# Kernel tuning notes

Measured on AMD Instinct MI355X. Metric: run time of the kernel, lower is better.

Reference implementation:

```python
import jax, jax.numpy as jnp
import numpy as np

N = 8192      # nodes
D_IN = 128    # input features
D_H = 48      # GAT hidden (hardcoded in module)
D_OUT = 32    # control output dim
NEG_INF = -9e15  # matches torch code's -9000000000000000.0


def setup_inputs() -> dict:
    key = jax.random.key(0)
    ks = jax.random.split(key, 12)
    s = 0.05
    return {
        "x": jax.random.normal(ks[0], (N, D_IN), jnp.float32),
        "adj": jax.random.randint(ks[1], (N, N), 0, 2, jnp.int32),
        "W_gat": jax.random.normal(ks[2], (D_H, D_IN), jnp.float32) * s,
        "a": jax.random.normal(ks[3], (1, D_H), jnp.float32) * s,
        "gamma": jnp.ones((D_H,), jnp.float32),
        "beta": jnp.zeros((D_H,), jnp.float32),
        "W1": jax.random.normal(ks[4], (256, D_H), jnp.float32) * s,
        "b1": jnp.zeros((256,), jnp.float32),
        "W2": jax.random.normal(ks[5], (128, 256), jnp.float32) * s,
        "b2": jnp.zeros((128,), jnp.float32),
        "W3": jax.random.normal(ks[6], (D_OUT, 128), jnp.float32) * s,
        "b3": jnp.zeros((D_OUT,), jnp.float32),
    }


def reference(x, adj, W_gat, a, gamma, beta, W1, b1, W2, b2, W3, b3):
    # --- LightweightGATLayer ---
    Wh = x @ W_gat.T                      # [N, D_H]
    s = Wh @ a.T                          # [N, 1] additive attention scores
    e = s + s.T                           # [N, N]
    e = jnp.where(e > 0, e, 0.2 * e)      # LeakyReLU(0.2)
    e = jnp.where(adj > 0, e, NEG_INF)    # mask non-edges
    attn = jax.nn.softmax(e, axis=1)      # row softmax; dropout is identity in eval
    h_prime = attn @ Wh                   # [N, D_H]
    # LayerNorm over last dim, eps=1e-5
    mu = jnp.mean(h_prime, axis=-1, keepdims=True)
    var = jnp.var(h_prime, axis=-1, keepdims=True)
    h = (h_prime - mu) * jax.lax.rsqrt(var + 1e-5) * gamma + beta
    # --- BiACT MLP head: 48 -> 256 -> 128 -> D_OUT ---
    h = jax.nn.relu(h @ W1.T + b1)
    h = jax.nn.relu(h @ W2.T + b2)
    return h @ W3.T + b3                  # [N, D_OUT]
```

## Files before the change

### kernel.cpp

```cpp
#include <hip/hip_runtime.h>

#define N 8192
#define DIN 128
#define DH 48
#define MT 128
#define KC 64
#define PSTR (KC + 8)
#define NSPLIT 8
#define JSPAN (N / NSPLIT)
#define NCHUNK (JSPAN / KC)
#define ACC_STRIDE 64
#define RB 32

typedef _Float16 half8 __attribute__((ext_vector_type(8)));
typedef float f32x4 __attribute__((ext_vector_type(4)));

__global__ __launch_bounds__(256) void k_wh(const float* __restrict__ x,
                                            const float* __restrict__ Wg,
                                            float* __restrict__ Wh) {
    __shared__ float wT[DIN * DH];
    int t = threadIdx.x;
    for (int e = t; e < DIN * DH; e += 256) {
        int c = e / DIN, k = e % DIN;
        wT[k * DH + c] = Wg[e];
    }
    __syncthreads();
    int o = blockIdx.x * 256 + t;
    int r = o / DH, c = o % DH;
    const float4* xr = (const float4*)(x + (size_t)r * DIN);
    float acc = 0.f;
    #pragma unroll 8
    for (int k4 = 0; k4 < DIN / 4; ++k4) {
        float4 xv = xr[k4];
        int kb = k4 * 4;
        acc += xv.x * wT[(kb + 0) * DH + c];
        acc += xv.y * wT[(kb + 1) * DH + c];
        acc += xv.z * wT[(kb + 2) * DH + c];
        acc += xv.w * wT[(kb + 3) * DH + c];
    }
    Wh[o] = acc;
}

__global__ __launch_bounds__(256) void k_s(const float* __restrict__ Wh,
                                           const float* __restrict__ a,
                                           float* __restrict__ s) {
    int r = blockIdx.x * 256 + threadIdx.x;
    const float4* wr = (const float4*)(Wh + (size_t)r * DH);
    const float4* av = (const float4*)a;
    float acc = 0.f;
    #pragma unroll
    for (int k4 = 0; k4 < DH / 4; ++k4) {
        float4 w = wr[k4]; float4 aa = av[k4];
        acc += w.x * aa.x + w.y * aa.y + w.z * aa.z + w.w * aa.w;
    }
    s[r] = acc;
}

__global__ __launch_bounds__(256) void k_gat(const int* __restrict__ adj,
                                             const float* __restrict__ Wh,
                                             const float* __restrict__ s,
                                             float* __restrict__ accWs) {
    __shared__ _Float16 pS[MT][PSTR];
    __shared__ _Float16 wS[64][PSTR];
    __shared__ float sRow[MT];
    int t = threadIdx.x;
    int tile = blockIdx.x & 63;
    int split = blockIdx.x >> 6;
    int i0 = tile * MT;
    int jbase = split * JSPAN;

    int lane = t & 63, w = t >> 6;
    int ln16 = lane & 15, kq = lane >> 4;
    int jp = t & 31, rg = t >> 5;

    const int* adjBase = adj + (size_t)(i0 + rg * 16) * N + jbase + 2 * jp;

    int2 adjR[16];
    float whR[12];
    #pragma unroll
    for (int it = 0; it < 16; ++it)
        adjR[it] = *(const int2*)(adjBase + (size_t)it * N);
    #pragma unroll
    for (int k = 0; k < 12; ++k)
        whR[k] = Wh[(size_t)jbase * DH + t + k * 256];

    if (t < MT) sRow[t] = s[i0 + t];
    for (int e = t; e < 16 * PSTR; e += 256) {
        int n = 48 + e / PSTR, k = e % PSTR;
        wS[n][k] = (n == 48) ? (_Float16)1.0f : (_Float16)0.0f;
    }

    f32x4 acc[2][4];
    #pragma unroll
    for (int a0 = 0; a0 < 2; ++a0)
        #pragma unroll
        for (int b0 = 0; b0 < 4; ++b0) acc[a0][b0] = (f32x4){0.f, 0.f, 0.f, 0.f};

    __syncthreads();

    for (int chunk = 0; chunk < NCHUNK; ++chunk) {
        int j0 = jbase + chunk * KC;
        #pragma unroll
        for (int k = 0; k < 12; ++k) {
            int e = t + k * 256;
            int jc = e / DH, d = e % DH;
            wS[d][jc] = (_Float16)whR[k];
        }
        {
            float2 sj = *(const float2*)(s + j0 + 2 * jp);
            #pragma unroll
            for (int it = 0; it < 16; ++it) {
                int r = rg * 16 + it;
                int2 av = adjR[it];
                float e0 = sRow[r] + sj.x;
                float e1 = sRow[r] + sj.y;
                e0 = fmaxf(e0, 0.2f * e0);
                e1 = fmaxf(e1, 0.2f * e1);
                float p0 = av.x ? __expf(e0) : 0.f;
                float p1 = av.y ? __expf(e1) : 0.f;
                union { _Float16 h[2]; unsigned u; } pk;
                pk.h[0] = (_Float16)p0;
                pk.h[1] = (_Float16)p1;
                *(unsigned*)&pS[r][2 * jp] = pk.u;
            }
        }
        if (chunk < NCHUNK - 1) {
            int jn = j0 + KC;
            #pragma unroll
            for (int it = 0; it < 16; ++it)
                adjR[it] = *(const int2*)(adjBase + (size_t)it * N + (chunk + 1) * KC);
            #pragma unroll
            for (int k = 0; k < 12; ++k)
                whR[k] = Wh[(size_t)jn * DH + t + k * 256];
        }
        __syncthreads();
        {
            const int m0 = w * 32;
            #pragma unroll
            for (int kt = 0; kt < 2; ++kt) {
                const int kk = kt * 32 + kq * 8;
                half8 b[4];
                #pragma unroll
                for (int nt = 0; nt < 4; ++nt)
                    b[nt] = *(const half8*)&wS[nt * 16 + ln16][kk];
                #pragma unroll
                for (int mtl = 0; mtl < 2; ++mtl) {
                    half8 a = *(const half8*)&pS[m0 + mtl * 16 + ln16][kk];
                    #pragma unroll
                    for (int nt = 0; nt < 4; ++nt)
                        acc[mtl][nt] = __builtin_amdgcn_mfma_f32_16x16x32_f16(
                            a, b[nt], acc[mtl][nt], 0, 0, 0);
                }
            }
        }
        __syncthreads();
    }
    size_t rbase = (size_t)split * N + i0;
    #pragma unroll
    for (int mtl = 0; mtl < 2; ++mtl) {
        #pragma unroll
        for (int nt = 0; nt < 4; ++nt) {
            int col = nt * 16 + ln16;
            if (nt == 3 && ln16 != 0) continue;
            #pragma unroll
            for (int reg = 0; reg < 4; ++reg) {
                int row = w * 32 + mtl * 16 + kq * 4 + reg;
                accWs[(rbase + row) * ACC_STRIDE + col] = acc[mtl][nt][reg];
            }
        }
    }
}

__global__ __launch_bounds__(256) void k_mlp(const float* __restrict__ accWs,
                                             const float* __restrict__ gamma,
                                             const float* __restrict__ beta,
                                             const float* __restrict__ W1, const float* __restrict__ b1,
                                             const float* __restrict__ W2, const float* __restrict__ b2,
                                             const float* __restrict__ W3, const float* __restrict__ b3,
                                             float* __restrict__ out) {
    __shared__ float hacc[RB * 49];
    __shared__ _Float16 hN[RB * 72];
    __shared__ _Float16 h1[RB * 264];
    __shared__ float h2[RB * 132];
    int t = threadIdx.x;
    int r0 = blockIdx.x * RB;
    int lane = t & 63, w = t >> 6;
    int ln16 = lane & 15, kq = lane >> 4;

    for (int e = t; e < RB * 49; e += 256) {
        int r = e / 49, d = e % 49;
        size_t base = (size_t)(r0 + r) * ACC_STRIDE + d;
        float v = 0.f;
        #pragma unroll
        for (int sp = 0; sp < NSPLIT; ++sp)
            v += accWs[(size_t)sp * N * ACC_STRIDE + base];
        hacc[e] = v;
    }
    __syncthreads();

    if (t < RB) {
        float invl = 1.f / hacc[t * 49 + 48];
        float sum = 0.f;
        for (int d = 0; d < DH; ++d) sum += hacc[t * 49 + d];
        float mean = sum * invl * (1.f / DH);
        float var = 0.f;
        for (int d = 0; d < DH; ++d) {
            float dv = hacc[t * 49 + d] * invl - mean;
            var += dv * dv;
        }
        var *= (1.f / DH);
        float rs = rsqrtf(var + 1e-5f);
        for (int d = 0; d < DH; ++d) {
            float hv = (hacc[t * 49 + d] * invl - mean) * rs;
            hN[t * 72 + d] = (_Float16)(hv * gamma[d] + beta[d]);
        }
        for (int d = DH; d < 72; ++d) hN[t * 72 + d] = (_Float16)0.f;
    }
    __syncthreads();

    {
        f32x4 acc1[2][4];
        #pragma unroll
        for (int mt = 0; mt < 2; ++mt)
            #pragma unroll
            for (int nt = 0; nt < 4; ++nt) acc1[mt][nt] = (f32x4){0.f, 0.f, 0.f, 0.f};
        #pragma unroll
        for (int kt = 0; kt < 2; ++kt) {
            int k = kt * 32 + kq * 8;
            half8 a[2];
            #pragma unroll
            for (int mt = 0; mt < 2; ++mt)
                a[mt] = *(const half8*)&hN[(mt * 16 + ln16) * 72 + k];
            #pragma unroll
            for (int ntl = 0; ntl < 4; ++ntl) {
                int n = (w * 4 + ntl) * 16 + ln16;
                half8 b;
                #pragma unroll
                for (int i = 0; i < 8; ++i) b[i] = (_Float16)0.f;
                if (k < DH) {
                    float4 lo = *(const float4*)(W1 + n * DH + k);
                    float4 hi = *(const float4*)(W1 + n * DH + k + 4);
                    b[0] = (_Float16)lo.x; b[1] = (_Float16)lo.y;
                    b[2] = (_Float16)lo.z; b[3] = (_Float16)lo.w;
                    b[4] = (_Float16)hi.x; b[5] = (_Float16)hi.y;
                    b[6] = (_Float16)hi.z; b[7] = (_Float16)hi.w;
                }
                #pragma unroll
                for (int mt = 0; mt < 2; ++mt)
                    acc1[mt][ntl] = __builtin_amdgcn_mfma_f32_16x16x32_f16(
                        a[mt], b, acc1[mt][ntl], 0, 0, 0);
            }
        }
        #pragma unroll
        for (int mt = 0; mt < 2; ++mt)
            #pragma unroll
            for (int ntl = 0; ntl < 4; ++ntl) {
                int col = (w * 4 + ntl) * 16 + ln16;
                float bias = b1[col];
                #pragma unroll
                for (int reg = 0; reg < 4; ++reg) {
                    int row = mt * 16 + kq * 4 + reg;
                    float v = acc1[mt][ntl][reg] + bias;
                    h1[row * 264 + col] = (_Float16)fmaxf(v, 0.f);
                }
            }
    }
    __syncthreads();

    {
        f32x4 acc2[2][2];
        #pragma unroll
        for (int mt = 0; mt < 2; ++mt)
            #pragma unroll
            for (int nt = 0; nt < 2; ++nt) acc2[mt][nt] = (f32x4){0.f, 0.f, 0.f, 0.f};
        #pragma unroll
        for (int kt = 0; kt < 8; ++kt) {
            int k = kt * 32 + kq * 8;
            half8 a[2];
            #pragma unroll
            for (int mt = 0; mt < 2; ++mt)
                a[mt] = *(const half8*)&h1[(mt * 16 + ln16) * 264 + k];
            #pragma unroll
            for (int ntl = 0; ntl < 2; ++ntl) {
                int n = (w * 2 + ntl) * 16 + ln16;
                float4 lo = *(const float4*)(W2 + n * 256 + k);
                float4 hi = *(const float4*)(W2 + n * 256 + k + 4);
                half8 b;
                b[0] = (_Float16)lo.x; b[1] = (_Float16)lo.y;
                b[2] = (_Float16)lo.z; b[3] = (_Float16)lo.w;
                b[4] = (_Float16)hi.x; b[5] = (_Float16)hi.y;
                b[6] = (_Float16)hi.z; b[7] = (_Float16)hi.w;
                #pragma unroll
                for (int mt = 0; mt < 2; ++mt)
                    acc2[mt][ntl] = __builtin_amdgcn_mfma_f32_16x16x32_f16(
                        a[mt], b, acc2[mt][ntl], 0, 0, 0);
            }
        }
        #pragma unroll
        for (int mt = 0; mt < 2; ++mt)
            #pragma unroll
            for (int ntl = 0; ntl < 2; ++ntl) {
                int col = (w * 2 + ntl) * 16 + ln16;
                float bias = b2[col];
                #pragma unroll
                for (int reg = 0; reg < 4; ++reg) {
                    int row = mt * 16 + kq * 4 + reg;
                    h2[row * 132 + col] = fmaxf(acc2[mt][ntl][reg] + bias, 0.f);
                }
            }
    }
    __syncthreads();

    {
        int c = t & 31;
        int g = t >> 5;
        int rb = g * 4;
        float acc[4];
        float bias = b3[c];
        #pragma unroll
        for (int r = 0; r < 4; ++r) acc[r] = bias;
        const float4* wrow = (const float4*)(W3 + c * 128);
        for (int k4 = 0; k4 < 32; ++k4) {
            float4 wv = wrow[k4];
            #pragma unroll
            for (int r = 0; r < 4; ++r) {
                const float4 hv = *(const float4*)(&h2[(rb + r) * 132 + k4 * 4]);
                acc[r] += wv.x * hv.x + wv.y * hv.y + wv.z * hv.z + wv.w * hv.w;
            }
        }
        #pragma unroll
        for (int r = 0; r < 4; ++r)
            out[(size_t)(r0 + rb + r) * 32 + c] = acc[r];
    }
}

extern "C" void kernel_launch(void* const* d_in, const int* in_sizes, int n_in,
                              void* d_out, int out_size, void* d_ws, size_t ws_size,
                              hipStream_t stream) {
    const float* x     = (const float*)d_in[0];
    const int*   adj   = (const int*)d_in[1];
    const float* Wg    = (const float*)d_in[2];
    const float* a     = (const float*)d_in[3];
    const float* gamma = (const float*)d_in[4];
    const float* beta  = (const float*)d_in[5];
    const float* W1    = (const float*)d_in[6];
    const float* b1    = (const float*)d_in[7];
    const float* W2    = (const float*)d_in[8];
    const float* b2    = (const float*)d_in[9];
    const float* W3    = (const float*)d_in[10];
    const float* b3    = (const float*)d_in[11];
    float* out = (float*)d_out;

    float* ws = (float*)d_ws;
    float* Wh    = ws;
    float* s     = ws + (size_t)N * DH;
    float* accWs = s + N;

    k_wh<<<N * DH / 256, 256, 0, stream>>>(x, Wg, Wh);
    k_s<<<N / 256, 256, 0, stream>>>(Wh, a, s);
    k_gat<<<64 * NSPLIT, 256, 0, stream>>>(adj, Wh, s, accWs);
    k_mlp<<<N / RB, 256, 0, stream>>>(accWs, gamma, beta, W1, b1, W2, b2, W3, b3, out);
}
```

Baseline: 467.0 us.

## Make GAT waves independent using a pre-transposed fp16 Wh and no block barriers

A new kernel writes Wh transposed to fp16, padded to 64 feature rows, with a row of ones that yields the softmax denominator. The GAT kernel now loads its MFMA B fragments straight from global memory instead of staging them in shared memory. Each wave computes and reads only its own 32 rows of attention probabilities, so both per-chunk __syncthreads are gone. The j-dimension split is doubled to 16 and launch bounds request 3 blocks per CU, for more parallelism and better latency hiding. The cost is an extra launch, redundant B-fragment loads per wave, and a partial-sum workspace and reduction in the MLP kernel that are twice as large.

```diff
diff --git a/kernel.cpp b/kernel.cpp
--- a/kernel.cpp
+++ b/kernel.cpp
@@ -6,7 +6,7 @@
 #define MT 128
 #define KC 64
 #define PSTR (KC + 8)
-#define NSPLIT 8
+#define NSPLIT 16
 #define JSPAN (N / NSPLIT)
 #define NCHUNK (JSPAN / KC)
 #define ACC_STRIDE 64
@@ -56,12 +56,22 @@
     s[r] = acc;
 }
 
-__global__ __launch_bounds__(256) void k_gat(const int* __restrict__ adj,
-                                             const float* __restrict__ Wh,
-                                             const float* __restrict__ s,
-                                             float* __restrict__ accWs) {
+__global__ __launch_bounds__(256) void k_tr(const float* __restrict__ Wh,
+                                            _Float16* __restrict__ WhT16) {
+    int o = blockIdx.x * 256 + threadIdx.x;
+    int d = o >> 13, j = o & 8191;
+    _Float16 v;
+    if (d < DH)       v = (_Float16)Wh[(size_t)j * DH + d];
+    else if (d == DH) v = (_Float16)1.0f;
+    else              v = (_Float16)0.0f;
+    WhT16[o] = v;
+}
+
+__global__ __launch_bounds__(256, 3) void k_gat(const int* __restrict__ adj,
+                                                const _Float16* __restrict__ WhT16,
+                                                const float* __restrict__ s,
+                                                float* __restrict__ accWs) {
     __shared__ _Float16 pS[MT][PSTR];
-    __shared__ _Float16 wS[64][PSTR];
     __shared__ float sRow[MT];
     int t = threadIdx.x;
     int tile = blockIdx.x & 63;
@@ -71,24 +81,17 @@
 
     int lane = t & 63, w = t >> 6;
     int ln16 = lane & 15, kq = lane >> 4;
-    int jp = t & 31, rg = t >> 5;
-
-    const int* adjBase = adj + (size_t)(i0 + rg * 16) * N + jbase + 2 * jp;
+    int jp = lane & 31, rh = lane >> 5;
+
+    int rw = w * 32;
+    const int* adjBase = adj + (size_t)(i0 + rw + rh * 16) * N + jbase + 2 * jp;
+
+    if (lane < 32) sRow[rw + lane] = s[i0 + rw + lane];
 
     int2 adjR[16];
-    float whR[12];
     #pragma unroll
     for (int it = 0; it < 16; ++it)
         adjR[it] = *(const int2*)(adjBase + (size_t)it * N);
-    #pragma unroll
-    for (int k = 0; k < 12; ++k)
-        whR[k] = Wh[(size_t)jbase * DH + t + k * 256];
-
-    if (t < MT) sRow[t] = s[i0 + t];
-    for (int e = t; e < 16 * PSTR; e += 256) {
-        int n = 48 + e / PSTR, k = e % PSTR;
-        wS[n][k] = (n == 48) ? (_Float16)1.0f : (_Float16)0.0f;
-    }
 
     f32x4 acc[2][4];
     #pragma unroll
@@ -96,21 +99,20 @@
         #pragma unroll
         for (int b0 = 0; b0 < 4; ++b0) acc[a0][b0] = (f32x4){0.f, 0.f, 0.f, 0.f};
 
-    __syncthreads();
-
     for (int chunk = 0; chunk < NCHUNK; ++chunk) {
         int j0 = jbase + chunk * KC;
-        #pragma unroll
-        for (int k = 0; k < 12; ++k) {
-            int e = t + k * 256;
-            int jc = e / DH, d = e % DH;
-            wS[d][jc] = (_Float16)whR[k];
-        }
+        half8 bf[2][4];
+        #pragma unroll
+        for (int kt = 0; kt < 2; ++kt)
+            #pragma unroll
+            for (int nt = 0; nt < 4; ++nt)
+                bf[kt][nt] = *(const half8*)&WhT16[(size_t)(nt * 16 + ln16) * N
+                                                  + j0 + kt * 32 + kq * 8];
         {
             float2 sj = *(const float2*)(s + j0 + 2 * jp);
             #pragma unroll
             for (int it = 0; it < 16; ++it) {
-                int r = rg * 16 + it;
+                int r = rw + rh * 16 + it;
                 int2 av = adjR[it];
                 float e0 = sRow[r] + sj.x;
                 float e1 = sRow[r] + sj.y;
@@ -125,35 +127,22 @@
             }
         }
         if (chunk < NCHUNK - 1) {
-            int jn = j0 + KC;
             #pragma unroll
             for (int it = 0; it < 16; ++it)
                 adjR[it] = *(const int2*)(adjBase + (size_t)it * N + (chunk + 1) * KC);
-            #pragma unroll
-            for (int k = 0; k < 12; ++k)
-                whR[k] = Wh[(size_t)jn * DH + t + k * 256];
-        }
-        __syncthreads();
-        {
-            const int m0 = w * 32;
-            #pragma unroll
-            for (int kt = 0; kt < 2; ++kt) {
-                const int kk = kt * 32 + kq * 8;
-                half8 b[4];
+        }
+        #pragma unroll
+        for (int kt = 0; kt < 2; ++kt) {
+            const int kk = kt * 32 + kq * 8;
+            #pragma unroll
+            for (int mtl = 0; mtl < 2; ++mtl) {
+                half8 a = *(const half8*)&pS[rw + mtl * 16 + ln16][kk];
                 #pragma unroll
                 for (int nt = 0; nt < 4; ++nt)
-                    b[nt] = *(const half8*)&wS[nt * 16 + ln16][kk];
-                #pragma unroll
-                for (int mtl = 0; mtl < 2; ++mtl) {
-                    half8 a = *(const half8*)&pS[m0 + mtl * 16 + ln16][kk];
-                    #pragma unroll
-                    for (int nt = 0; nt < 4; ++nt)
-                        acc[mtl][nt] = __builtin_amdgcn_mfma_f32_16x16x32_f16(
-                            a, b[nt], acc[mtl][nt], 0, 0, 0);
-                }
-            }
-        }
-        __syncthreads();
+                    acc[mtl][nt] = __builtin_amdgcn_mfma_f32_16x16x32_f16(
+                        a, bf[kt][nt], acc[mtl][nt], 0, 0, 0);
+            }
+        }
     }
     size_t rbase = (size_t)split * N + i0;
     #pragma unroll
@@ -164,7 +153,7 @@
             if (nt == 3 && ln16 != 0) continue;
             #pragma unroll
             for (int reg = 0; reg < 4; ++reg) {
-                int row = w * 32 + mtl * 16 + kq * 4 + reg;
+                int row = rw + mtl * 16 + kq * 4 + reg;
                 accWs[(rbase + row) * ACC_STRIDE + col] = acc[mtl][nt][reg];
             }
         }
@@ -352,12 +341,14 @@
     float* out = (float*)d_out;
 
     float* ws = (float*)d_ws;
-    float* Wh    = ws;
-    float* s     = ws + (size_t)N * DH;
-    float* accWs = s + N;
+    float* Wh       = ws;
+    float* s        = ws + (size_t)N * DH;
+    _Float16* WhT16 = (_Float16*)(s + N);
+    float* accWs    = (float*)((char*)WhT16 + (size_t)64 * N * sizeof(_Float16));
 
     k_wh<<<N * DH / 256, 256, 0, stream>>>(x, Wg, Wh);
     k_s<<<N / 256, 256, 0, stream>>>(Wh, a, s);
-    k_gat<<<64 * NSPLIT, 256, 0, stream>>>(adj, Wh, s, accWs);
+    k_tr<<<64 * N / 256, 256, 0, stream>>>(Wh, WhT16);
+    k_gat<<<64 * NSPLIT, 256, 0, stream>>>(adj, WhT16, s, accWs);
     k_mlp<<<N / RB, 256, 0, stream>>>(accWs, gamma, beta, W1, b1, W2, b2, W3, b3, out);
 }
```

Result: faster. 456.3 us (-2.3%).
